# Kernel tuning notes

Hardware: AMD Instinct MI355X
Metric: run time of the kernel (lower is better)

The kernel has to match this reference:

```python
import jax, jax.numpy as jnp
import numpy as np

EXPAND = 1
N_CHUNKS = 6
CHUNK = 4

def setup_inputs() -> dict:
    key = jax.random.key(0)
    k1, k2 = jax.random.split(key)
    B = 4_000_000
    pre = jax.random.normal(k1, (B, 25), dtype=jnp.float32)
    tar = jax.random.uniform(k2, (B, 25), dtype=jnp.float32)
    return {"pre": pre, "tar": tar}

def reference(pre, tar):
    B = pre.shape[0]
    # 6 chunks of 4: softmax over each chunk, scaled by 3*expand.
    chunks = pre[:, :N_CHUNKS * CHUNK].reshape(B, N_CHUNKS, CHUNK)
    out24 = 3.0 * EXPAND * jax.nn.softmax(chunks, axis=-1)  # [B,6,4]
    tar24 = tar[:, :N_CHUNKS * CHUNK].reshape(B, N_CHUNKS, CHUNK)
    # out[24] = relu(pre[24]) is computed in the original but never enters the
    # loss (loss uses out[0:24] only), so it is omitted.
    per_sample = jnp.mean(jnp.abs(out24 - tar24), axis=(1, 2))  # mean over 24 elems
    return jnp.sum(per_sample)
```

## Files before the change

kernel.cpp:

```cpp
#include <hip/hip_runtime.h>

#define THREADS 256
#define ROWS_PER_BLOCK 256
#define ROW 25
#define TILE_FLOATS (ROWS_PER_BLOCK * ROW)
#define TILE_VEC4 (TILE_FLOATS / 4)

__launch_bounds__(THREADS)
__global__ void loss_soft_add_kernel(const float* __restrict__ pre,
                                     const float* __restrict__ tar,
                                     float* __restrict__ out, int B) {
    __shared__ float s_pre[TILE_FLOATS];
    __shared__ float s_tar[TILE_FLOATS];
    __shared__ float s_part[THREADS / 64];

    const int tid  = threadIdx.x;
    const int row0 = blockIdx.x * ROWS_PER_BLOCK;
    const int nrows = min(ROWS_PER_BLOCK, B - row0);
    const int nfloats = nrows * ROW;

    const size_t base = (size_t)row0 * ROW;

    if (nfloats == TILE_FLOATS) {
        const float4* gp = (const float4*)(pre + base);
        const float4* gt = (const float4*)(tar + base);
        float4* sp = (float4*)s_pre;
        float4* st = (float4*)s_tar;
        #pragma unroll
        for (int k = 0; k < (TILE_VEC4 + THREADS - 1) / THREADS; ++k) {
            int idx = tid + k * THREADS;
            if (idx < TILE_VEC4) {
                sp[idx] = gp[idx];
                st[idx] = gt[idx];
            }
        }
    } else {
        for (int idx = tid; idx < nfloats; idx += THREADS) {
            s_pre[idx] = pre[base + idx];
            s_tar[idx] = tar[base + idx];
        }
    }
    __syncthreads();

    float acc = 0.0f;
    if (tid < nrows) {
        const float* rp = &s_pre[tid * ROW];
        const float* rt = &s_tar[tid * ROW];
        float total = 0.0f;
        #pragma unroll
        for (int c = 0; c < 6; ++c) {
            float x0 = rp[c * 4 + 0];
            float x1 = rp[c * 4 + 1];
            float x2 = rp[c * 4 + 2];
            float x3 = rp[c * 4 + 3];
            float m = fmaxf(fmaxf(x0, x1), fmaxf(x2, x3));
            float e0 = __expf(x0 - m);
            float e1 = __expf(x1 - m);
            float e2 = __expf(x2 - m);
            float e3 = __expf(x3 - m);
            float k = 3.0f / (e0 + e1 + e2 + e3);
            total += fabsf(e0 * k - rt[c * 4 + 0]);
            total += fabsf(e1 * k - rt[c * 4 + 1]);
            total += fabsf(e2 * k - rt[c * 4 + 2]);
            total += fabsf(e3 * k - rt[c * 4 + 3]);
        }
        acc = total * (1.0f / 24.0f);
    }

    #pragma unroll
    for (int off = 32; off > 0; off >>= 1)
        acc += __shfl_down(acc, off, 64);
    const int wid = tid >> 6, lane = tid & 63;
    if (lane == 0) s_part[wid] = acc;
    __syncthreads();
    if (tid == 0) {
        float bsum = s_part[0] + s_part[1] + s_part[2] + s_part[3];
        atomicAdd(out, bsum);
    }
}

extern "C" void kernel_launch(void* const* d_in, const int* in_sizes, int n_in,
                              void* d_out, int out_size, void* d_ws, size_t ws_size,
                              hipStream_t stream) {
    const float* pre = (const float*)d_in[0];
    const float* tar = (const float*)d_in[1];
    float* out = (float*)d_out;
    const int B = in_sizes[0] / ROW;

    hipMemsetAsync(d_out, 0, sizeof(float) * out_size, stream);

    const int blocks = (B + ROWS_PER_BLOCK - 1) / ROWS_PER_BLOCK;
    loss_soft_add_kernel<<<blocks, THREADS, 0, stream>>>(pre, tar, out, B);
}
```

Baseline: 794.8 us.

## Stage pre via direct global-to-LDS loads and stream tar from global

Loads the pre tile into LDS with the async global_load_lds builtin, which bypasses registers. The softmax results are written back in place, and tar is then read straight from global memory as coalesced float4s, with the column-24 entries masked out. This halves the LDS footprint, which together with a launch-bounds occupancy hint is meant to raise occupancy and cut LDS traffic. The cost is an extra barrier, per-element modulo masking, and reliance on the direct-to-LDS load path being correct and well-aligned.

```diff
diff --git a/kernel.cpp b/kernel.cpp
--- a/kernel.cpp
+++ b/kernel.cpp
@@ -5,67 +5,91 @@
 #define ROW 25
 #define TILE_FLOATS (ROWS_PER_BLOCK * ROW)
 #define TILE_VEC4 (TILE_FLOATS / 4)
+#define FULL_K (TILE_VEC4 / THREADS)
 
-__launch_bounds__(THREADS)
+__device__ __forceinline__ void load16_to_lds(const float* g, float* l) {
+    __builtin_amdgcn_global_load_lds(
+        (const __attribute__((address_space(1))) void*)g,
+        (__attribute__((address_space(3))) void*)l,
+        16, 0, 0);
+}
+
+__launch_bounds__(THREADS, 6)
 __global__ void loss_soft_add_kernel(const float* __restrict__ pre,
                                      const float* __restrict__ tar,
                                      float* __restrict__ out, int B) {
-    __shared__ float s_pre[TILE_FLOATS];
-    __shared__ float s_tar[TILE_FLOATS];
+    __shared__ __attribute__((aligned(16))) float s_pre[TILE_FLOATS];
     __shared__ float s_part[THREADS / 64];
 
     const int tid  = threadIdx.x;
     const int row0 = blockIdx.x * ROWS_PER_BLOCK;
     const int nrows = min(ROWS_PER_BLOCK, B - row0);
     const int nfloats = nrows * ROW;
-
     const size_t base = (size_t)row0 * ROW;
 
     if (nfloats == TILE_FLOATS) {
-        const float4* gp = (const float4*)(pre + base);
-        const float4* gt = (const float4*)(tar + base);
-        float4* sp = (float4*)s_pre;
-        float4* st = (float4*)s_tar;
+        const float* gp = pre + base;
         #pragma unroll
-        for (int k = 0; k < (TILE_VEC4 + THREADS - 1) / THREADS; ++k) {
-            int idx = tid + k * THREADS;
-            if (idx < TILE_VEC4) {
-                sp[idx] = gp[idx];
-                st[idx] = gt[idx];
-            }
+        for (int k = 0; k < FULL_K; ++k) {
+            const int idx = tid + k * THREADS;
+            load16_to_lds(gp + idx * 4, &s_pre[idx * 4]);
+        }
+        if (tid < TILE_VEC4 - FULL_K * THREADS) {
+            const int idx = tid + FULL_K * THREADS;
+            load16_to_lds(gp + idx * 4, &s_pre[idx * 4]);
         }
     } else {
-        for (int idx = tid; idx < nfloats; idx += THREADS) {
+        for (int idx = tid; idx < nfloats; idx += THREADS)
             s_pre[idx] = pre[base + idx];
-            s_tar[idx] = tar[base + idx];
+    }
+    __syncthreads();
+
+    if (tid < nrows) {
+        float* rp = &s_pre[tid * ROW];
+        #pragma unroll
+        for (int c = 0; c < 6; ++c) {
+            const float x0 = rp[c * 4 + 0];
+            const float x1 = rp[c * 4 + 1];
+            const float x2 = rp[c * 4 + 2];
+            const float x3 = rp[c * 4 + 3];
+            const float m = fmaxf(fmaxf(x0, x1), fmaxf(x2, x3));
+            const float e0 = __expf(x0 - m);
+            const float e1 = __expf(x1 - m);
+            const float e2 = __expf(x2 - m);
+            const float e3 = __expf(x3 - m);
+            const float k3 = 3.0f / (e0 + e1 + e2 + e3);
+            rp[c * 4 + 0] = e0 * k3;
+            rp[c * 4 + 1] = e1 * k3;
+            rp[c * 4 + 2] = e2 * k3;
+            rp[c * 4 + 3] = e3 * k3;
         }
     }
     __syncthreads();
 
     float acc = 0.0f;
-    if (tid < nrows) {
-        const float* rp = &s_pre[tid * ROW];
-        const float* rt = &s_tar[tid * ROW];
-        float total = 0.0f;
+    if (nfloats == TILE_FLOATS) {
+        const float4* st = (const float4*)(tar + base);
+        const float4* so = (const float4*)s_pre;
         #pragma unroll
-        for (int c = 0; c < 6; ++c) {
-            float x0 = rp[c * 4 + 0];
-            float x1 = rp[c * 4 + 1];
-            float x2 = rp[c * 4 + 2];
-            float x3 = rp[c * 4 + 3];
-            float m = fmaxf(fmaxf(x0, x1), fmaxf(x2, x3));
-            float e0 = __expf(x0 - m);
-            float e1 = __expf(x1 - m);
-            float e2 = __expf(x2 - m);
-            float e3 = __expf(x3 - m);
-            float k = 3.0f / (e0 + e1 + e2 + e3);
-            total += fabsf(e0 * k - rt[c * 4 + 0]);
-            total += fabsf(e1 * k - rt[c * 4 + 1]);
-            total += fabsf(e2 * k - rt[c * 4 + 2]);
-            total += fabsf(e3 * k - rt[c * 4 + 3]);
+        for (int k = 0; k <= FULL_K; ++k) {
+            const int idx = tid + k * THREADS;
+            if (idx < TILE_VEC4) {
+                const float4 t = st[idx];
+                const float4 o = so[idx];
+                unsigned col = (unsigned)(idx * 4) % 25u;
+                acc += (col == 24u) ? 0.0f : fabsf(o.x - t.x); col = (col == 24u) ? 0u : col + 1u;
+                acc += (col == 24u) ? 0.0f : fabsf(o.y - t.y); col = (col == 24u) ? 0u : col + 1u;
+                acc += (col == 24u) ? 0.0f : fabsf(o.z - t.z); col = (col == 24u) ? 0u : col + 1u;
+                acc += (col == 24u) ? 0.0f : fabsf(o.w - t.w);
+            }
         }
-        acc = total * (1.0f / 24.0f);
+    } else {
+        for (int i = tid; i < nfloats; i += THREADS) {
+            if ((unsigned)i % 25u != 24u)
+                acc += fabsf(s_pre[i] - tar[base + i]);
+        }
     }
+    acc *= (1.0f / 24.0f);
 
     #pragma unroll
     for (int off = 32; off > 0; off >>= 1)
@@ -74,7 +98,7 @@
     if (lane == 0) s_part[wid] = acc;
     __syncthreads();
     if (tid == 0) {
-        float bsum = s_part[0] + s_part[1] + s_part[2] + s_part[3];
+        const float bsum = s_part[0] + s_part[1] + s_part[2] + s_part[3];
         atomicAdd(out, bsum);
     }
 }
```

New measurement: 796.3 us. No clear change (+0.2%).
